# Kernel tuning notes

Measured on AMD Instinct MI355X. Metric: run time of the kernel, lower is better.

## Reference

```python
import jax, jax.numpy as jnp
import numpy as np

B, S, D = 1, 2048, 4096
H, HKV, HD = 32, 8, 128
MAX_SEQ = 4096
EPS = 1e-5


def rmsnorm(x, w, eps=EPS):
    var = jnp.mean(x * x, axis=-1, keepdims=True)
    return w * (x * jax.lax.rsqrt(var + eps))


def rotate_half_interleaved(x):
    x1 = x[..., ::2]
    x2 = x[..., 1::2]
    return jnp.stack((-x2, x1), axis=-1).reshape(x.shape)


def setup_inputs() -> dict:
    key = jax.random.key(0)
    ks = jax.random.split(key, 8)
    hidden_states = jax.random.normal(ks[0], (B, S, D), dtype=jnp.float32)
    # realistic interleaved RoPE tables: each frequency repeated twice along head_dim
    inv_freq = 1.0 / (10000.0 ** (np.arange(0, HD, 2, dtype=np.float32) / HD))
    pos = np.arange(S, dtype=np.float32)
    ang = pos[:, None] * inv_freq[None, :]            # [S, HD/2]
    ang = np.repeat(ang, 2, axis=-1)                   # [S, HD] interleaved
    cos = jnp.asarray(np.cos(ang))[None].repeat(B, axis=0)  # [B, S, HD]
    sin = jnp.asarray(np.sin(ang))[None].repeat(B, axis=0)
    scale = 1.0 / np.sqrt(D)
    return {
        "hidden_states": hidden_states,
        "cos": cos,
        "sin": sin,
        "k_cache": jnp.zeros((B, MAX_SEQ, HKV, HD), dtype=jnp.float32),
        "v_cache": jnp.zeros((B, MAX_SEQ, HKV, HD), dtype=jnp.float32),
        "Wq": jax.random.normal(ks[1], (D, H * HD), dtype=jnp.float32) * scale,
        "Wk": jax.random.normal(ks[2], (D, HKV * HD), dtype=jnp.float32) * scale,
        "Wv": jax.random.normal(ks[3], (D, HKV * HD), dtype=jnp.float32) * scale,
        "Wo": jax.random.normal(ks[4], (H * HD, D), dtype=jnp.float32) * scale,
        "rms_weight": jnp.ones((D,), dtype=jnp.float32),
        "position_ids": jnp.arange(S, dtype=jnp.int64 if jax.config.jax_enable_x64 else jnp.int32),
        "seq_len": S,
    }


def reference(hidden_states, cos, sin, k_cache, v_cache, Wq, Wk, Wv, Wo,
              rms_weight, position_ids, seq_len):
    residual = hidden_states
    h = rmsnorm(hidden_states, rms_weight)
    b, s = h.shape[:2]

    q = jnp.einsum('bsd,de->bse', h, Wq).reshape(b, s, H, HD)
    k = jnp.einsum('bsd,de->bse', h, Wk).reshape(b, s, HKV, HD)
    v = jnp.einsum('bsd,de->bse', h, Wv).reshape(b, s, HKV, HD)

    # interleaved RoPE, cos/sin broadcast over head axis (unsqueeze_dim=-2)
    c = cos[:, :, None, :]
    si = sin[:, :, None, :]
    q = q * c + rotate_half_interleaved(q) * si
    k = k * c + rotate_half_interleaved(k) * si

    # KV-cache scatter at position_ids (repeat_factor == 1 here)
    k_cache_new = k_cache.at[:, position_ids].set(k)
    v_cache_new = v_cache.at[:, position_ids].set(v)

    # prefill path (new_tok_seq_len > 1): causal SDPA with GQA over fresh K/V
    group = H // HKV
    k_full = jnp.repeat(k, group, axis=2)  # [b, s, H, HD]
    v_full = jnp.repeat(v, group, axis=2)
    qh = q.transpose(0, 2, 1, 3)           # bhqd
    kh = k_full.transpose(0, 2, 1, 3)
    vh = v_full.transpose(0, 2, 1, 3)
    scores = jnp.einsum('bhqd,bhkd->bhqk', qh, kh) / jnp.sqrt(jnp.float32(HD))
    causal = jnp.tril(jnp.ones((s, s), dtype=bool))
    scores = jnp.where(causal[None, None], scores, jnp.finfo(scores.dtype).min)
    probs = jax.nn.softmax(scores, axis=-1)
    attn = jnp.einsum('bhqk,bhkd->bhqd', probs, vh)
    attn = attn.transpose(0, 2, 1, 3).reshape(b, s, H * HD)

    out = jnp.einsum('bse,ed->bsd', attn, Wo)
    with_residual = residual + out
    return with_residual, k_cache_new, v_cache_new
```

## Files before the change

kernel.cpp:

```cpp
#include <hip/hip_runtime.h>
#include <hip/hip_bf16.h>
#include <cstdint>

#define S_LEN 2048
#define DMODEL 4096
#define NHEAD 32
#define NKV 8
#define HDIM 128
#define MAXSEQ 4096
#define NQKV 6144

typedef __bf16 bf16x8 __attribute__((ext_vector_type(8)));
typedef float f32x4 __attribute__((ext_vector_type(4)));
typedef short s16x4 __attribute__((ext_vector_type(4)));

__device__ __forceinline__ short f2bf(float f) {
  unsigned u = __builtin_bit_cast(unsigned, f);
  u += 0x7fffu + ((u >> 16) & 1u);
  return (short)(u >> 16);
}

__device__ __forceinline__ void gload_lds16(const void* g, const void* l) {
  __builtin_amdgcn_global_load_lds((const __attribute__((address_space(1))) unsigned*)g,
                                   (__attribute__((address_space(3))) unsigned*)(l), 16, 0, 0);
}

__global__ __launch_bounds__(256) void rmsnorm_kernel(const float* __restrict__ x,
                                                      const float* __restrict__ w,
                                                      short* __restrict__ out) {
  const int row = blockIdx.x, tid = threadIdx.x;
  const float4* xr = (const float4*)(x + (size_t)row * DMODEL);
  const float4* wr = (const float4*)w;
  float4 v[4];
  float ss = 0.f;
#pragma unroll
  for (int i = 0; i < 4; ++i) {
    v[i] = xr[tid + i * 256];
    ss += v[i].x * v[i].x + v[i].y * v[i].y + v[i].z * v[i].z + v[i].w * v[i].w;
  }
#pragma unroll
  for (int m = 32; m; m >>= 1) ss += __shfl_down(ss, m, 64);
  __shared__ float red[4];
  if ((tid & 63) == 0) red[tid >> 6] = ss;
  __syncthreads();
  float tot = red[0] + red[1] + red[2] + red[3];
  float sc = rsqrtf(tot * (1.f / DMODEL) + 1e-5f);
#pragma unroll
  for (int i = 0; i < 4; ++i) {
    float4 wv = wr[tid + i * 256];
    s16x4 o;
    o[0] = f2bf(v[i].x * sc * wv.x);
    o[1] = f2bf(v[i].y * sc * wv.y);
    o[2] = f2bf(v[i].z * sc * wv.z);
    o[3] = f2bf(v[i].w * sc * wv.w);
    *(s16x4*)&out[(size_t)row * DMODEL + (size_t)(tid + i * 256) * 4] = o;
  }
}

__global__ __launch_bounds__(256) void cast_transpose(const float* __restrict__ src,
                                                      short* __restrict__ dst,
                                                      int rows, int cols) {
  __shared__ float tile[32][33];
  const int c0 = blockIdx.x * 32, r0 = blockIdx.y * 32;
  const int tx = threadIdx.x, ty = threadIdx.y;
#pragma unroll
  for (int i = ty; i < 32; i += 8) tile[i][tx] = src[(size_t)(r0 + i) * cols + c0 + tx];
  __syncthreads();
  const int tid = ty * 32 + tx;
#pragma unroll
  for (int rep = 0; rep < 2; ++rep) {
    int w = rep * 256 + tid;
    int i = w >> 4, pr = (w & 15) * 2;
    short2 o;
    o.x = f2bf(tile[pr][i]);
    o.y = f2bf(tile[pr + 1][i]);
    *(short2*)&dst[(size_t)(c0 + i) * rows + r0 + pr] = o;
  }
}

__global__ __launch_bounds__(256) void v_transpose(const float* __restrict__ QKV,
                                                   float* __restrict__ vc,
                                                   short* __restrict__ vt) {
  __shared__ float tile[32][33];
  const int d0 = blockIdx.x * 32, s0 = blockIdx.y * 32, g = blockIdx.z;
  const int tx = threadIdx.x, ty = threadIdx.y;
#pragma unroll
  for (int i = ty; i < 32; i += 8) {
    float v = QKV[(size_t)(s0 + i) * NQKV + (NHEAD + NKV) * HDIM + g * HDIM + d0 + tx];
    tile[i][tx] = v;
    vc[(size_t)(s0 + i) * (NKV * HDIM) + g * HDIM + d0 + tx] = v;
  }
  __syncthreads();
  const int tid = ty * 32 + tx;
#pragma unroll
  for (int rep = 0; rep < 2; ++rep) {
    int w = rep * 256 + tid;
    int i = w >> 4, pr = (w & 15) * 2;
    short2 o;
    o.x = f2bf(tile[pr][i]);
    o.y = f2bf(tile[pr + 1][i]);
    *(short2*)&vt[((size_t)g * HDIM + d0 + i) * S_LEN + s0 + pr] = o;
  }
}

__global__ __launch_bounds__(256, 2) void gemm_bt(const short* __restrict__ A,
                                                  const short* __restrict__ Bt,
                                                  float* __restrict__ C,
                                                  const float* __restrict__ resid,
                                                  int M, int N, int K) {
  __shared__ __align__(16) short As[128 * 64];
  __shared__ __align__(16) short Bs[128 * 64];
  const int tid = threadIdx.x;
  const int lane = tid & 63, wave = tid >> 6;
  const int wr = wave >> 1, wc = wave & 1;
  const int lrow = lane & 15, quad = lane >> 4;
  const int m0 = blockIdx.y * 128, n0 = blockIdx.x * 128;
  f32x4 acc[4][4] = {};
  for (int k0 = 0; k0 < K; k0 += 64) {
#pragma unroll
    for (int c = 0; c < 4; ++c) {
      int idx = (wave * 4 + c) * 512 + lane * 8;
      int row = idx >> 6, kc = idx & 63;
      gload_lds16(A + (size_t)(m0 + row) * K + k0 + kc, &As[(wave * 4 + c) * 512]);
      gload_lds16(Bt + (size_t)(n0 + row) * K + k0 + kc, &Bs[(wave * 4 + c) * 512]);
    }
    __syncthreads();
#pragma unroll
    for (int kk = 0; kk < 2; ++kk) {
      bf16x8 af[4], bfr[4];
#pragma unroll
      for (int i = 0; i < 4; ++i)
        af[i] = *(const bf16x8*)&As[(wr * 64 + i * 16 + lrow) * 64 + kk * 32 + quad * 8];
#pragma unroll
      for (int j = 0; j < 4; ++j)
        bfr[j] = *(const bf16x8*)&Bs[(wc * 64 + j * 16 + lrow) * 64 + kk * 32 + quad * 8];
#pragma unroll
      for (int i = 0; i < 4; ++i)
#pragma unroll
        for (int j = 0; j < 4; ++j)
          acc[i][j] = __builtin_amdgcn_mfma_f32_16x16x32_bf16(af[i], bfr[j], acc[i][j], 0, 0, 0);
    }
    __syncthreads();
  }
#pragma unroll
  for (int i = 0; i < 4; ++i)
#pragma unroll
    for (int j = 0; j < 4; ++j) {
      int row = m0 + wr * 64 + i * 16 + quad * 4;
      int col = n0 + wc * 64 + j * 16 + lrow;
#pragma unroll
      for (int r = 0; r < 4; ++r) {
        float v = acc[i][j][r];
        size_t o = (size_t)(row + r) * N + col;
        if (resid) v += resid[o];
        C[o] = v;
      }
    }
}

__global__ __launch_bounds__(256) void rope_kernel(const float* __restrict__ QKV,
                                                   const float* __restrict__ cosb,
                                                   const float* __restrict__ sinb,
                                                   short* __restrict__ qo,
                                                   short* __restrict__ ko,
                                                   float* __restrict__ kc,
                                                   float* __restrict__ vc) {
  const int s = blockIdx.x, tid = threadIdx.x;
  const float4* r4 = (const float4*)(QKV + (size_t)s * NQKV);
  const float qscale = 0.08838834764831845f;
#pragma unroll
  for (int it = 0; it < 5; ++it) {
    int i = it * 256 + tid;
    float4 x = r4[i];
    int e = i * 4;
    int d = e & 127;
    float4 c = *(const float4*)&cosb[(size_t)s * HDIM + d];
    float4 si = *(const float4*)&sinb[(size_t)s * HDIM + d];
    float o0 = x.x * c.x - x.y * si.x;
    float o1 = x.y * c.y + x.x * si.y;
    float o2 = x.z * c.z - x.w * si.z;
    float o3 = x.w * c.w + x.z * si.w;
    if (e < NHEAD * HDIM) {
      int hh = e >> 7;
      s16x4 ov;
      ov[0] = f2bf(o0 * qscale); ov[1] = f2bf(o1 * qscale);
      ov[2] = f2bf(o2 * qscale); ov[3] = f2bf(o3 * qscale);
      *(s16x4*)&qo[((size_t)hh * S_LEN + s) * HDIM + d] = ov;
    } else {
      int ek = e - NHEAD * HDIM;
      int g = ek >> 7;
      s16x4 ov;
      ov[0] = f2bf(o0); ov[1] = f2bf(o1); ov[2] = f2bf(o2); ov[3] = f2bf(o3);
      *(s16x4*)&ko[((size_t)g * S_LEN + s) * HDIM + d] = ov;
      *(float4*)&kc[(size_t)s * (NKV * HDIM) + ek] = make_float4(o0, o1, o2, o3);
    }
  }
  {
    const size_t base = (size_t)S_LEN * NKV * HDIM;
    const size_t i = (size_t)s * 256 + tid;
    const float4 z = make_float4(0.f, 0.f, 0.f, 0.f);
    ((float4*)(kc + base))[i] = z;
    ((float4*)(vc + base))[i] = z;
  }
}

#define TKEY 128
__global__ __launch_bounds__(256, 1) void attn_kernel(const short* __restrict__ Q,
                                                      const short* __restrict__ Kb,
                                                      const short* __restrict__ Vt,
                                                      short* __restrict__ out) {
  extern __shared__ __align__(16) short smem[];
  short* Ks = smem;
  short* Vs = smem + 32768;
  short* Ps = smem + 65536;
  const int tid = threadIdx.x;
  const int lane = tid & 63, wave = tid >> 6;
  const int lrow = lane & 15, quad = lane >> 4;
  const int g = blockIdx.x & 7, p = blockIdx.x >> 3;
  const int h = g * 4 + wave;
  const float L2E = 1.44269504f;
  const short* Kg = Kb + (size_t)g * S_LEN * HDIM;
  const short* Vg = Vt + (size_t)g * HDIM * S_LEN;
  short* Pw = Ps + wave * 1024;

#pragma unroll 1
  for (int ph = 0; ph < 2; ++ph) {
    const int qt = ph ? (63 - p) : p;
    const int nt = (qt >> 2) + 1;

    bf16x8 qf[2][4];
#pragma unroll
    for (int i = 0; i < 2; ++i)
#pragma unroll
      for (int kf = 0; kf < 4; ++kf)
        qf[i][kf] = *(const bf16x8*)&Q[((size_t)h * S_LEN + qt * 32 + i * 16 + lrow) * HDIM + kf * 32 + quad * 8];

    f32x4 O[2][8] = {};
    float mrun[2][4], lrun[2][4];
#pragma unroll
    for (int i = 0; i < 2; ++i)
#pragma unroll
      for (int r = 0; r < 4; ++r) { mrun[i][r] = -1e30f; lrun[i][r] = 0.f; }

#pragma unroll
    for (int ii = 0; ii < 8; ++ii) {
      int s = (wave * 8 + ii) * 64 + lane;
      int r = s >> 4, gg = (s & 15) ^ (r & 15);
      gload_lds16(Kg + (size_t)r * HDIM + gg * 8, Ks + (wave * 8 + ii) * 512);
    }
#pragma unroll
    for (int ii = 0; ii < 8; ++ii) {
      int s = (wave * 8 + ii) * 64 + lane;
      int d = s >> 4, kg = (s & 15) ^ (d & 15);
      gload_lds16(Vg + (size_t)d * S_LEN + kg * 8, Vs + (wave * 8 + ii) * 512);
    }
    __syncthreads();

#pragma unroll 1
    for (int t = 0; t < nt; ++t) {
      const int bsel = t & 1;
      if (t + 1 < nt) {
        const int kb2 = (t + 1) * TKEY, o = (1 - bsel) * 16384;
#pragma unroll
        for (int ii = 0; ii < 8; ++ii) {
          int s = (wave * 8 + ii) * 64 + lane;
          int r = s >> 4, gg = (s & 15) ^ (r & 15);
          gload_lds16(Kg + (size_t)(kb2 + r) * HDIM + gg * 8, Ks + o + (wave * 8 + ii) * 512);
        }
#pragma unroll
        for (int ii = 0; ii < 8; ++ii) {
          int s = (wave * 8 + ii) * 64 + lane;
          int d = s >> 4, kg = (s & 15) ^ (d & 15);
          gload_lds16(Vg + (size_t)d * S_LEN + kb2 + kg * 8, Vs + o + (wave * 8 + ii) * 512);
        }
      }
      const short* Kc = Ks + bsel * 16384;
      const short* Vc = Vs + bsel * 16384;

      f32x4 sc[2][8] = {};
#pragma unroll
      for (int c = 0; c < 8; ++c) {
        int r = c * 16 + lrow;
#pragma unroll
        for (int kf = 0; kf < 4; ++kf) {
          int slot = r * 16 + ((kf * 4 + quad) ^ lrow);
          bf16x8 kfr = *(const bf16x8*)&Kc[slot * 8];
          sc[0][c] = __builtin_amdgcn_mfma_f32_16x16x32_bf16(qf[0][kf], kfr, sc[0][c], 0, 0, 0);
          sc[1][c] = __builtin_amdgcn_mfma_f32_16x16x32_bf16(qf[1][kf], kfr, sc[1][c], 0, 0, 0);
        }
      }

      const int kb = t * TKEY;
      const bool last = (t == nt - 1);
#pragma unroll
      for (int i = 0; i < 2; ++i) {
        if (last) {
#pragma unroll
          for (int c = 0; c < 8; ++c) {
            int key = kb + c * 16 + lrow;
#pragma unroll
            for (int r = 0; r < 4; ++r) {
              int row = qt * 32 + i * 16 + quad * 4 + r;
              if (key > row) sc[i][c][r] = -1e30f;
            }
          }
        }
        float tm[4];
#pragma unroll
        for (int r = 0; r < 4; ++r) tm[r] = sc[i][0][r];
#pragma unroll
        for (int c = 1; c < 8; ++c)
#pragma unroll
          for (int r = 0; r < 4; ++r) tm[r] = fmaxf(tm[r], sc[i][c][r]);
#pragma unroll
        for (int msk = 1; msk <= 8; msk <<= 1)
#pragma unroll
          for (int r = 0; r < 4; ++r) tm[r] = fmaxf(tm[r], __shfl_xor(tm[r], msk, 64));
#pragma unroll
        for (int r = 0; r < 4; ++r) {
          float nm = fmaxf(mrun[i][r], tm[r]);
          float alpha = exp2f((mrun[i][r] - nm) * L2E);
          mrun[i][r] = nm;
          lrun[i][r] *= alpha;
#pragma unroll
          for (int jd = 0; jd < 8; ++jd) O[i][jd][r] *= alpha;
        }
        float rs[4] = {0.f, 0.f, 0.f, 0.f};
#pragma unroll
        for (int c = 0; c < 8; ++c)
#pragma unroll
          for (int r = 0; r < 4; ++r) {
            float pv = exp2f((sc[i][c][r] - mrun[i][r]) * L2E);
            sc[i][c][r] = pv;
            rs[r] += pv;
          }
#pragma unroll
        for (int msk = 1; msk <= 8; msk <<= 1)
#pragma unroll
          for (int r = 0; r < 4; ++r) rs[r] += __shfl_xor(rs[r], msk, 64);
#pragma unroll
        for (int r = 0; r < 4; ++r) lrun[i][r] += rs[r];
      }

#pragma unroll
      for (int ks = 0; ks < 4; ++ks) {
#pragma unroll
        for (int i = 0; i < 2; ++i)
#pragma unroll
          for (int cc = 0; cc < 2; ++cc) {
            int c = ks * 2 + cc;
            int kg = cc * 2 + (lrow >> 3), off = lrow & 7;
#pragma unroll
            for (int r = 0; r < 4; ++r) {
              int q2 = i * 16 + quad * 4 + r;
              int slot = q2 * 4 + (kg ^ (q2 & 3) ^ ((q2 >> 2) & 3));
              Pw[slot * 8 + off] = f2bf(sc[i][c][r]);
            }
          }
        bf16x8 pa[2];
#pragma unroll
        for (int i = 0; i < 2; ++i) {
          int q2 = i * 16 + lrow;
          int slot = q2 * 4 + (quad ^ (q2 & 3) ^ ((q2 >> 2) & 3));
          pa[i] = *(const bf16x8*)&Pw[slot * 8];
        }
#pragma unroll
        for (int jd = 0; jd < 8; ++jd) {
          int d = jd * 16 + lrow;
          int slotv = d * 16 + ((ks * 4 + quad) ^ lrow);
          bf16x8 vb = *(const bf16x8*)&Vc[slotv * 8];
          O[0][jd] = __builtin_amdgcn_mfma_f32_16x16x32_bf16(pa[0], vb, O[0][jd], 0, 0, 0);
          O[1][jd] = __builtin_amdgcn_mfma_f32_16x16x32_bf16(pa[1], vb, O[1][jd], 0, 0, 0);
        }
      }
      __syncthreads();
    }

#pragma unroll
    for (int i = 0; i < 2; ++i)
#pragma unroll
      for (int r = 0; r < 4; ++r) {
        float inv = 1.f / lrun[i][r];
        int row = qt * 32 + i * 16 + quad * 4 + r;
#pragma unroll
        for (int jd = 0; jd < 8; ++jd)
          out[(size_t)row * DMODEL + h * HDIM + jd * 16 + lrow] = f2bf(O[i][jd][r] * inv);
      }
    __syncthreads();
  }
}

extern "C" void kernel_launch(void* const* d_in, const int* in_sizes, int n_in,
                              void* d_out, int out_size, void* d_ws, size_t ws_size,
                              hipStream_t stream) {
  const float* hs   = (const float*)d_in[0];
  const float* cosb = (const float*)d_in[1];
  const float* sinb = (const float*)d_in[2];
  const float* Wq   = (const float*)d_in[5];
  const float* Wk   = (const float*)d_in[6];
  const float* Wv   = (const float*)d_in[7];
  const float* Wo   = (const float*)d_in[8];
  const float* rmsw = (const float*)d_in[9];

  float* outp = (float*)d_out;
  float* kc = outp + (size_t)S_LEN * DMODEL;
  float* vc = kc + (size_t)MAXSEQ * NKV * HDIM;

  char* p = (char*)d_ws;
  short* h_bf  = (short*)p; p += (size_t)S_LEN * DMODEL * 2;
  short* WqkvT = (short*)p; p += (size_t)NQKV * DMODEL * 2;
  short* WoT   = (short*)p; p += (size_t)DMODEL * DMODEL * 2;
  float* QKV   = (float*)p; p += (size_t)S_LEN * NQKV * 4;
  short* q_bf  = (short*)p; p += (size_t)NHEAD * S_LEN * HDIM * 2;
  short* k_bf  = (short*)p; p += (size_t)NKV * S_LEN * HDIM * 2;
  short* vt_bf = (short*)p; p += (size_t)NKV * HDIM * S_LEN * 2;
  short* attn_bf = h_bf;

  const int ATTN_LDS = 139264;
  hipFuncSetAttribute(reinterpret_cast<const void*>(attn_kernel),
                      hipFuncAttributeMaxDynamicSharedMemorySize, ATTN_LDS);

  rmsnorm_kernel<<<S_LEN, 256, 0, stream>>>(hs, rmsw, h_bf);
  cast_transpose<<<dim3(DMODEL / 32, DMODEL / 32), dim3(32, 8), 0, stream>>>(Wq, WqkvT, DMODEL, DMODEL);
  cast_transpose<<<dim3(1024 / 32, DMODEL / 32), dim3(32, 8), 0, stream>>>(Wk, WqkvT + (size_t)DMODEL * DMODEL, DMODEL, 1024);
  cast_transpose<<<dim3(1024 / 32, DMODEL / 32), dim3(32, 8), 0, stream>>>(Wv, WqkvT + (size_t)5120 * DMODEL, DMODEL, 1024);
  cast_transpose<<<dim3(DMODEL / 32, DMODEL / 32), dim3(32, 8), 0, stream>>>(Wo, WoT, DMODEL, DMODEL);
  gemm_bt<<<dim3(NQKV / 128, S_LEN / 128), 256, 0, stream>>>(h_bf, WqkvT, QKV, nullptr, S_LEN, NQKV, DMODEL);
  rope_kernel<<<S_LEN, 256, 0, stream>>>(QKV, cosb, sinb, q_bf, k_bf, kc, vc);
  v_transpose<<<dim3(HDIM / 32, S_LEN / 32, NKV), dim3(32, 8), 0, stream>>>(QKV, vc, vt_bf);
  attn_kernel<<<256, 256, ATTN_LDS, stream>>>(q_bf, k_bf, vt_bf, attn_bf);
  gemm_bt<<<dim3(DMODEL / 128, S_LEN / 128), 256, 0, stream>>>(attn_bf, WoT, outp, hs, S_LEN, DMODEL, DMODEL);
}
```

Baseline: 663.1 us.

## Replace 128x128 GEMM with 256x256 double-buffered, swizzled, phase-pipelined GEMM

```diff
diff --git a/kernel.cpp b/kernel.cpp
--- a/kernel.cpp
+++ b/kernel.cpp
@@ -103,59 +103,125 @@
   }
 }
 
-__global__ __launch_bounds__(256, 2) void gemm_bt(const short* __restrict__ A,
+
+template<int KS, int MH>
+__device__ __forceinline__ void ph_load(const short* __restrict__ AsH, const short* __restrict__ BsH,
+                                        const int lrow, const int quad, const int brow0,
+                                        bf16x8 (&aR)[4], bf16x8 (&bR)[2][4]) {
+  const int xr = lrow & 7;
+#pragma unroll
+  for (int f = 0; f < 4; ++f)
+    aR[f] = *(const bf16x8*)&AsH[((((MH * 4 + f) * 16 + lrow) * 8) + ((KS * 4 + quad) ^ xr)) * 8];
+  if constexpr (KS == 0 && MH == 0) {
+#pragma unroll
+    for (int ks = 0; ks < 2; ++ks)
+#pragma unroll
+      for (int f = 0; f < 4; ++f)
+        bR[ks][f] = *(const bf16x8*)&BsH[(((brow0 + f * 16 + lrow) * 8) + ((ks * 4 + quad) ^ xr)) * 8];
+  }
+}
+
+template<int KS, int MH>
+__device__ __forceinline__ void ph_mfma(bf16x8 (&aR)[4], bf16x8 (&bR)[2][4], f32x4 (&acc)[8][4]) {
+#pragma unroll
+  for (int f = 0; f < 4; ++f)
+#pragma unroll
+    for (int n = 0; n < 4; ++n)
+      acc[MH * 4 + f][n] =
+          __builtin_amdgcn_mfma_f32_16x16x32_bf16(aR[f], bR[KS][n], acc[MH * 4 + f][n], 0, 0, 0);
+}
+
+__global__ __launch_bounds__(512, 2) void gemm256(const short* __restrict__ A,
                                                   const short* __restrict__ Bt,
                                                   float* __restrict__ C,
                                                   const float* __restrict__ resid,
                                                   int M, int N, int K) {
-  __shared__ __align__(16) short As[128 * 64];
-  __shared__ __align__(16) short Bs[128 * 64];
+  extern __shared__ __align__(16) short smem[];
+  short* As = smem;
+  short* Bs = smem + 32768;
   const int tid = threadIdx.x;
   const int lane = tid & 63, wave = tid >> 6;
-  const int wr = wave >> 1, wc = wave & 1;
+  const int wm = wave >> 2, wn = wave & 3;
   const int lrow = lane & 15, quad = lane >> 4;
-  const int m0 = blockIdx.y * 128, n0 = blockIdx.x * 128;
-  f32x4 acc[4][4] = {};
-  for (int k0 = 0; k0 < K; k0 += 64) {
-#pragma unroll
-    for (int c = 0; c < 4; ++c) {
-      int idx = (wave * 4 + c) * 512 + lane * 8;
-      int row = idx >> 6, kc = idx & 63;
-      gload_lds16(A + (size_t)(m0 + row) * K + k0 + kc, &As[(wave * 4 + c) * 512]);
-      gload_lds16(Bt + (size_t)(n0 + row) * K + k0 + kc, &Bs[(wave * 4 + c) * 512]);
-    }
-    __syncthreads();
-#pragma unroll
-    for (int kk = 0; kk < 2; ++kk) {
-      bf16x8 af[4], bfr[4];
-#pragma unroll
-      for (int i = 0; i < 4; ++i)
-        af[i] = *(const bf16x8*)&As[(wr * 64 + i * 16 + lrow) * 64 + kk * 32 + quad * 8];
-#pragma unroll
-      for (int j = 0; j < 4; ++j)
-        bfr[j] = *(const bf16x8*)&Bs[(wc * 64 + j * 16 + lrow) * 64 + kk * 32 + quad * 8];
-#pragma unroll
-      for (int i = 0; i < 4; ++i)
-#pragma unroll
-        for (int j = 0; j < 4; ++j)
-          acc[i][j] = __builtin_amdgcn_mfma_f32_16x16x32_bf16(af[i], bfr[j], acc[i][j], 0, 0, 0);
-    }
-    __syncthreads();
-  }
-#pragma unroll
-  for (int i = 0; i < 4; ++i)
-#pragma unroll
-    for (int j = 0; j < 4; ++j) {
-      int row = m0 + wr * 64 + i * 16 + quad * 4;
-      int col = n0 + wc * 64 + j * 16 + lrow;
+  const int bhalf = wn >> 1, brow0 = (wn & 1) * 64;
+  const int m0 = blockIdx.y * 256, n0 = blockIdx.x * 256;
+  const int srow = tid >> 3;
+  const int scol = ((tid & 7) ^ (srow & 7)) << 3;
+  const short* Ag = A + (size_t)m0 * K;
+  const short* Bg = Bt + (size_t)n0 * K;
+  const int nk = K >> 6;
+
+#define STAGE_A(b, h, kt) do { \
+    const short* g_ = Ag + (size_t)((h) * 128 + srow) * K + (size_t)(kt) * 64 + scol; \
+    short* l_ = As + ((b) * 2 + (h)) * 8192 + wave * 512; \
+    gload_lds16(g_, l_); \
+    gload_lds16(g_ + (size_t)64 * K, l_ + 4096); \
+  } while (0)
+#define STAGE_B(b, h, kt) do { \
+    const short* g_ = Bg + (size_t)((h) * 128 + srow) * K + (size_t)(kt) * 64 + scol; \
+    short* l_ = Bs + ((b) * 2 + (h)) * 8192 + wave * 512; \
+    gload_lds16(g_, l_); \
+    gload_lds16(g_ + (size_t)64 * K, l_ + 4096); \
+  } while (0)
+#define VW_NONE
+#define VW_4 asm volatile("s_waitcnt vmcnt(4)" ::: "memory");
+#define VW_COND if (more) { asm volatile("s_waitcnt vmcnt(4)" ::: "memory"); } \
+                else      { asm volatile("s_waitcnt vmcnt(0)" ::: "memory"); }
+#define PHASE(BUF, KS, MH, STMT, VW) \
+  ph_load<KS, MH>(As + ((BUF) * 2 + wm) * 8192, Bs + ((BUF) * 2 + bhalf) * 8192, \
+                  lrow, quad, brow0, aR, bR); \
+  STMT; \
+  VW \
+  __builtin_amdgcn_s_barrier(); \
+  asm volatile("s_waitcnt lgkmcnt(0)" ::: "memory"); \
+  __builtin_amdgcn_s_setprio(1); \
+  ph_mfma<KS, MH>(aR, bR, acc); \
+  __builtin_amdgcn_s_setprio(0); \
+  __builtin_amdgcn_s_barrier();
+
+  f32x4 acc[8][4] = {};
+  bf16x8 aR[4], bR[2][4];
+
+  STAGE_A(0, 0, 0); STAGE_A(0, 1, 0);
+  STAGE_B(0, 0, 0); STAGE_B(0, 1, 0);
+  STAGE_B(1, 0, 1); STAGE_B(1, 1, 1);
+  asm volatile("s_waitcnt vmcnt(4)" ::: "memory");
+  __builtin_amdgcn_s_barrier();
+
+  const int niter = nk >> 1;
+  for (int i = 0; i < niter; ++i) {
+    const int t = 2 * i;
+    const bool more = (t + 2 < nk);
+    PHASE(0, 0, 0, STAGE_A(1, 0, t + 1), VW_NONE)
+    PHASE(0, 0, 1, STAGE_A(1, 1, t + 1), VW_NONE)
+    PHASE(0, 1, 0, if (more) { STAGE_B(0, 0, t + 2); }, VW_NONE)
+    PHASE(0, 1, 1, if (more) { STAGE_B(0, 1, t + 2); }, VW_COND)
+    PHASE(1, 0, 0, if (more) { STAGE_A(0, 0, t + 2); }, VW_NONE)
+    PHASE(1, 0, 1, if (more) { STAGE_A(0, 1, t + 2); }, VW_NONE)
+    PHASE(1, 1, 0, if (more) { STAGE_B(1, 0, t + 3); }, VW_NONE)
+    PHASE(1, 1, 1, if (more) { STAGE_B(1, 1, t + 3); }, VW_4)
+  }
+
+#pragma unroll
+  for (int fm = 0; fm < 8; ++fm)
+#pragma unroll
+    for (int fn = 0; fn < 4; ++fn) {
+      int row = m0 + wm * 128 + fm * 16 + quad * 4;
+      int col = n0 + wn * 64 + fn * 16 + lrow;
 #pragma unroll
       for (int r = 0; r < 4; ++r) {
-        float v = acc[i][j][r];
+        float v = acc[fm][fn][r];
         size_t o = (size_t)(row + r) * N + col;
         if (resid) v += resid[o];
         C[o] = v;
       }
     }
+#undef STAGE_A
+#undef STAGE_B
+#undef VW_NONE
+#undef VW_4
+#undef VW_COND
+#undef PHASE
 }
 
 __global__ __launch_bounds__(256) void rope_kernel(const float* __restrict__ QKV,
@@ -419,15 +485,18 @@
   const int ATTN_LDS = 139264;
   hipFuncSetAttribute(reinterpret_cast<const void*>(attn_kernel),
                       hipFuncAttributeMaxDynamicSharedMemorySize, ATTN_LDS);
+  const int GEMM_LDS = 131072;
+  hipFuncSetAttribute(reinterpret_cast<const void*>(gemm256),
+                      hipFuncAttributeMaxDynamicSharedMemorySize, GEMM_LDS);
 
   rmsnorm_kernel<<<S_LEN, 256, 0, stream>>>(hs, rmsw, h_bf);
   cast_transpose<<<dim3(DMODEL / 32, DMODEL / 32), dim3(32, 8), 0, stream>>>(Wq, WqkvT, DMODEL, DMODEL);
   cast_transpose<<<dim3(1024 / 32, DMODEL / 32), dim3(32, 8), 0, stream>>>(Wk, WqkvT + (size_t)DMODEL * DMODEL, DMODEL, 1024);
   cast_transpose<<<dim3(1024 / 32, DMODEL / 32), dim3(32, 8), 0, stream>>>(Wv, WqkvT + (size_t)5120 * DMODEL, DMODEL, 1024);
   cast_transpose<<<dim3(DMODEL / 32, DMODEL / 32), dim3(32, 8), 0, stream>>>(Wo, WoT, DMODEL, DMODEL);
-  gemm_bt<<<dim3(NQKV / 128, S_LEN / 128), 256, 0, stream>>>(h_bf, WqkvT, QKV, nullptr, S_LEN, NQKV, DMODEL);
+  gemm256<<<dim3(NQKV / 256, S_LEN / 256), 512, GEMM_LDS, stream>>>(h_bf, WqkvT, QKV, nullptr, S_LEN, NQKV, DMODEL);
   rope_kernel<<<S_LEN, 256, 0, stream>>>(QKV, cosb, sinb, q_bf, k_bf, kc, vc);
   v_transpose<<<dim3(HDIM / 32, S_LEN / 32, NKV), dim3(32, 8), 0, stream>>>(QKV, vc, vt_bf);
   attn_kernel<<<256, 256, ATTN_LDS, stream>>>(q_bf, k_bf, vt_bf, attn_bf);
-  gemm_bt<<<dim3(DMODEL / 128, S_LEN / 128), 256, 0, stream>>>(attn_bf, WoT, outp, hs, S_LEN, DMODEL, DMODEL);
-}
+  gemm256<<<dim3(DMODEL / 256, S_LEN / 256), 512, GEMM_LDS, stream>>>(attn_bf, WoT, outp, hs, S_LEN, DMODEL, DMODEL);
+}
```

After: 675.3 us. No clear change (+1.8%).
